# Performance work log

Hardware: AMD Instinct MI355X
Metric: run time of the kernel (lower is better)

Reference implementation:

```python
import jax, jax.numpy as jnp
import numpy as np

N_NODES = 100000
N_EDGES = 3200000
N_GRAPHS = 64
IN_FEATS = 128
NUM_CLASSES = 10


def setup_inputs() -> dict:
    key = jax.random.key(0)
    ks = jax.random.split(key, 12)
    in_feat = jax.random.normal(ks[0], (N_NODES, IN_FEATS), dtype=jnp.float32)
    src = jax.random.randint(ks[1], (N_EDGES,), 0, N_NODES, dtype=jnp.int32)
    dst = jax.random.randint(ks[2], (N_EDGES,), 0, N_NODES, dtype=jnp.int32)
    graph_ids = jnp.sort(jax.random.randint(ks[3], (N_NODES,), 0, N_GRAPHS, dtype=jnp.int32))
    def glorot(k, fan_in, fan_out):
        s = jnp.sqrt(6.0 / (fan_in + fan_out))
        return jax.random.uniform(k, (fan_in, fan_out), jnp.float32, -s, s)
    W1 = glorot(ks[4], IN_FEATS, 64); b1 = jnp.zeros((64,), jnp.float32)
    W2 = glorot(ks[5], 64, 128);      b2 = jnp.zeros((128,), jnp.float32)
    W3 = glorot(ks[6], 128, 64);      b3 = jnp.zeros((64,), jnp.float32)
    Wd = glorot(ks[7], 64, NUM_CLASSES)
    bd = jnp.zeros((NUM_CLASSES,), jnp.float32)
    return {"in_feat": in_feat, "src": src, "dst": dst, "graph_ids": graph_ids,
            "W1": W1, "b1": b1, "W2": W2, "b2": b2, "W3": W3, "b3": b3,
            "Wd": Wd, "bd": bd}


def _graph_conv(h, src, dst, norm_src, norm_dst, W, b):
    # DGL GraphConv, norm='both': h' = D_in^{-1/2} A (D_out^{-1/2} h) W + b
    x = h * norm_src[:, None]
    m = jax.ops.segment_sum(x[src], dst, num_segments=N_NODES)
    m = m * norm_dst[:, None]
    return m @ W + b


def reference(in_feat, src, dst, graph_ids, W1, b1, W2, b2, W3, b3, Wd, bd):
    ones = jnp.ones((N_EDGES,), jnp.float32)
    deg_out = jax.ops.segment_sum(ones, src, num_segments=N_NODES)
    deg_in = jax.ops.segment_sum(ones, dst, num_segments=N_NODES)
    norm_src = jax.lax.rsqrt(jnp.clip(deg_out, 1.0))
    norm_dst = jax.lax.rsqrt(jnp.clip(deg_in, 1.0))

    h = jax.nn.relu(_graph_conv(in_feat, src, dst, norm_src, norm_dst, W1, b1))
    h = jax.nn.relu(_graph_conv(h, src, dst, norm_src, norm_dst, W2, b2))
    h = jax.nn.relu(_graph_conv(h, src, dst, norm_src, norm_dst, W3, b3))

    hg = jax.ops.segment_sum(h, graph_ids, num_segments=N_GRAPHS)  # [G, 64]
    hg = jnp.tanh(hg)
    return hg @ Wd + bd  # [G, num_classes]
```

## Files before the change

### kernel.cpp

```cpp
#include <hip/hip_runtime.h>
#include <hip/hip_bf16.h>


constexpr int NN = 100000;
constexpr int NE = 3200000;
constexpr int NG = 64;

constexpr int CBITS = 16;
constexpr int CHUNK = 1 << CBITS;
constexpr int NCHUNK = (NE + CHUNK - 1) / CHUNK;
constexpr int WORDS4 = NN / 8;

typedef __attribute__((ext_vector_type(8))) short short8;
typedef __attribute__((ext_vector_type(4))) float f32x4;
typedef __attribute__((ext_vector_type(2))) float f32x2;


__global__ __launch_bounds__(1024) void hist_kernel(
    const int* __restrict__ src, const int* __restrict__ dst,
    uint* __restrict__ pdst, uint* __restrict__ psrc,
    unsigned char* __restrict__ lrank) {
  __shared__ uint bins[WORDS4];
  for (int i = threadIdx.x; i < WORDS4; i += 1024) bins[i] = 0;
  __syncthreads();
  const int c = blockIdx.x;
  const int start = c << CBITS;
  const int end = min(start + CHUNK, NE);
  if (blockIdx.y == 0) {
    for (int i = start + threadIdx.x; i < end; i += 1024) {
      int n = dst[i];
      uint old = atomicAdd(&bins[n >> 3], 1u << ((n & 7) * 4));
      lrank[i] = (unsigned char)((old >> ((n & 7) * 4)) & 0xf);
    }
  } else {
    for (int i = start + threadIdx.x; i < end; i += 1024) {
      int n = src[i];
      atomicAdd(&bins[n >> 3], 1u << ((n & 7) * 4));
    }
  }
  __syncthreads();
  uint* pp = ((blockIdx.y == 0) ? pdst : psrc) + (size_t)c * WORDS4;
  for (int i = threadIdx.x; i < WORDS4; i += 1024) pp[i] = bins[i];
}


__global__ __launch_bounds__(256) void reduce2_kernel(
    const uint* __restrict__ pdst, const uint* __restrict__ psrc,
    unsigned char* __restrict__ Pb, int* __restrict__ deg_in,
    float* __restrict__ nd, float* __restrict__ ns, float* __restrict__ hg) {
  int w = blockIdx.x * 256 + threadIdx.x;
  uint run[8] = {0, 0, 0, 0, 0, 0, 0, 0};
  if (blockIdx.y == 0) {
    if (w >= WORDS4) return;
#pragma unroll 7
    for (int c = 0; c < NCHUNK; ++c) {
      uint lo = run[0] | (run[1] << 8) | (run[2] << 16) | (run[3] << 24);
      uint hi = run[4] | (run[5] << 8) | (run[6] << 16) | (run[7] << 24);
      ((uint2*)(Pb + (size_t)c * NN))[w] = make_uint2(lo, hi);
      uint v = pdst[(size_t)c * WORDS4 + w];
#pragma unroll
      for (int k = 0; k < 8; ++k) run[k] += (v >> (4 * k)) & 0xfu;
    }
    ((int4*)deg_in)[2 * w] = make_int4(run[0], run[1], run[2], run[3]);
    ((int4*)deg_in)[2 * w + 1] = make_int4(run[4], run[5], run[6], run[7]);
    float4 f0, f1;
    f0.x = rsqrtf(fmaxf((float)run[0], 1.f));
    f0.y = rsqrtf(fmaxf((float)run[1], 1.f));
    f0.z = rsqrtf(fmaxf((float)run[2], 1.f));
    f0.w = rsqrtf(fmaxf((float)run[3], 1.f));
    f1.x = rsqrtf(fmaxf((float)run[4], 1.f));
    f1.y = rsqrtf(fmaxf((float)run[5], 1.f));
    f1.z = rsqrtf(fmaxf((float)run[6], 1.f));
    f1.w = rsqrtf(fmaxf((float)run[7], 1.f));
    ((float4*)nd)[2 * w] = f0;
    ((float4*)nd)[2 * w + 1] = f1;
  } else {
    if (blockIdx.x == 0) {
      for (int k = threadIdx.x; k < 1024; k += 256)
        ((float4*)hg)[k] = make_float4(0.f, 0.f, 0.f, 0.f);
    }
    if (w >= WORDS4) return;
#pragma unroll 7
    for (int c = 0; c < NCHUNK; ++c) {
      uint v = psrc[(size_t)c * WORDS4 + w];
#pragma unroll
      for (int k = 0; k < 8; ++k) run[k] += (v >> (4 * k)) & 0xfu;
    }
    float4 f0, f1;
    f0.x = rsqrtf(fmaxf((float)run[0], 1.f));
    f0.y = rsqrtf(fmaxf((float)run[1], 1.f));
    f0.z = rsqrtf(fmaxf((float)run[2], 1.f));
    f0.w = rsqrtf(fmaxf((float)run[3], 1.f));
    f1.x = rsqrtf(fmaxf((float)run[4], 1.f));
    f1.y = rsqrtf(fmaxf((float)run[5], 1.f));
    f1.z = rsqrtf(fmaxf((float)run[6], 1.f));
    f1.w = rsqrtf(fmaxf((float)run[7], 1.f));
    ((float4*)ns)[2 * w] = f0;
    ((float4*)ns)[2 * w + 1] = f1;
  }
}


__device__ __forceinline__ uint pack_bf16(float a, float b) {
  uint ua = __float_as_uint(a), ub = __float_as_uint(b);
  ua = (ua + 0x7fffu + ((ua >> 16) & 1u)) >> 16;
  ub = (ub + 0x7fffu + ((ub >> 16) & 1u)) & 0xffff0000u;
  return ua | ub;
}

__device__ __forceinline__ ushort to_bf16(float a) {
  uint ua = __float_as_uint(a);
  return (ushort)((ua + 0x7fffu + ((ua >> 16) & 1u)) >> 16);
}

union U16 {
  uint4 u;
  short8 s;
};
__device__ __forceinline__ short8 as_short8(uint4 u) {
  U16 t;
  t.u = u;
  return t.s;
}

__device__ __forceinline__ f32x2 bf2(uint u) {
  f32x2 r;
  r.x = __uint_as_float(u << 16);
  r.y = __uint_as_float(u & 0xffff0000u);
  return r;
}

__device__ __forceinline__ void add8(f32x2* a, uint4 v) {
  a[0] += bf2(v.x);
  a[1] += bf2(v.y);
  a[2] += bf2(v.z);
  a[3] += bf2(v.w);
}


__global__ __launch_bounds__(256) void scan1t_kernel(
    const int* __restrict__ deg, int* __restrict__ row_off,
    int* __restrict__ bsums, int n, const float* __restrict__ W1,
    const float* __restrict__ W2, const float* __restrict__ W3,
    ushort* __restrict__ Wt1, ushort* __restrict__ Wt2,
    ushort* __restrict__ Wt3) {
  int gi = blockIdx.x * 256 + threadIdx.x;
  if (gi < 8192) {
    int nn = gi >> 7, k = gi & 127;
    Wt1[gi] = to_bf16(W1[k * 64 + nn]);
  } else if (gi < 16384) {
    int j = gi - 8192;
    int nn = j >> 6, k = j & 63;
    Wt2[j] = to_bf16(W2[k * 128 + nn]);
  } else if (gi < 24576) {
    int j = gi - 16384;
    int nn = j >> 7, k = j & 127;
    Wt3[j] = to_bf16(W3[k * 64 + nn]);
  }
  __shared__ int s[256];
  int t = threadIdx.x;
  int base = blockIdx.x * 1024 + t * 4;
  int v0 = 0, v1 = 0, v2 = 0, v3 = 0;
  if (base + 0 < n) v0 = deg[base + 0];
  if (base + 1 < n) v1 = deg[base + 1];
  if (base + 2 < n) v2 = deg[base + 2];
  if (base + 3 < n) v3 = deg[base + 3];
  int sum = v0 + v1 + v2 + v3;
  s[t] = sum;
  __syncthreads();
  for (int off = 1; off < 256; off <<= 1) {
    int x = (t >= off) ? s[t - off] : 0;
    __syncthreads();
    s[t] += x;
    __syncthreads();
  }
  int excl = s[t] - sum;
  if (t == 255) bsums[blockIdx.x] = s[255];
  if (base + 0 < n) row_off[base + 0] = excl;
  if (base + 1 < n) row_off[base + 1] = excl + v0;
  if (base + 2 < n) row_off[base + 2] = excl + v0 + v1;
  if (base + 3 < n) row_off[base + 3] = excl + v0 + v1 + v2;
}


__global__ __launch_bounds__(256) void scan23_kernel(
    int* __restrict__ row_off, const int* __restrict__ bsums, int nb, int n) {
  __shared__ int si[128], so[128];
  int t = threadIdx.x;
  if (t < 128) {
    int v = (t < nb) ? bsums[t] : 0;
    si[t] = v;
    so[t] = v;
  }
  __syncthreads();
  for (int off = 1; off < 128; off <<= 1) {
    int x = 0;
    if (t < 128 && t >= off) x = si[t - off];
    __syncthreads();
    if (t < 128) si[t] += x;
    __syncthreads();
  }
  int i = blockIdx.x * 256 + t;
  if (i < n) {
    int bk = i >> 10;
    row_off[i] += si[bk] - so[bk];
  }
  if (blockIdx.x == 0 && t == 0) row_off[n] = si[127];
}


__global__ __launch_bounds__(256) void fill_kernel(
    const int* __restrict__ src, const int* __restrict__ dst,
    const int* __restrict__ row_off, const unsigned char* __restrict__ Pb,
    const unsigned char* __restrict__ lrank, int* __restrict__ csr, int e) {
  int i = blockIdx.x * 256 + threadIdx.x;
  if (i < e) {
    int d = dst[i];
    int c = i >> CBITS;
    int pos = row_off[d] + (int)Pb[(size_t)c * NN + d] + (int)lrank[i];
    csr[pos] = src[i];
  }
}


__global__ __launch_bounds__(256) void gemm1_kernel(
    const float* __restrict__ A, const ushort* __restrict__ Wt,
    const float* __restrict__ scale, ushort* __restrict__ C, int n) {
  int wid = threadIdx.x >> 6, lane = threadIdx.x & 63;
  int r = lane & 15, quad = lane >> 4;
  int m16 = blockIdx.x * 64 + wid * 16;
  if (m16 >= n) return;
  int mc = min(m16 + r, n - 1);
  short8 a[4];
#pragma unroll
  for (int ks = 0; ks < 4; ++ks) {
    const float4* p = (const float4*)(A + (size_t)mc * 128 + ks * 32 + quad * 8);
    float4 x = p[0], y = p[1];
    uint4 u;
    u.x = pack_bf16(x.x, x.y);
    u.y = pack_bf16(x.z, x.w);
    u.z = pack_bf16(y.x, y.y);
    u.w = pack_bf16(y.z, y.w);
    a[ks] = as_short8(u);
  }
#pragma unroll
  for (int nt = 0; nt < 4; ++nt) {
    f32x4 acc = {0.f, 0.f, 0.f, 0.f};
#pragma unroll
    for (int ks = 0; ks < 4; ++ks) {
      short8 b = as_short8(
          *(const uint4*)(Wt + (size_t)(nt * 16 + r) * 128 + ks * 32 + quad * 8));
      acc = __builtin_amdgcn_mfma_f32_16x16x32_bf16(a[ks], b, acc, 0, 0, 0);
    }
#pragma unroll
    for (int reg = 0; reg < 4; ++reg) {
      int m = m16 + quad * 4 + reg;
      if (m < n) C[(size_t)m * 64 + nt * 16 + r] = to_bf16(acc[reg] * scale[m]);
    }
  }
}


__global__ __launch_bounds__(256) void gemm23_kernel(
    const ushort* __restrict__ m2, const ushort* __restrict__ Wt2,
    const float* __restrict__ b2, const float* __restrict__ ns,
    const ushort* __restrict__ Wt3, ushort* __restrict__ t3, int n) {
  __shared__ ushort sX[4][16][136];
  int wid = threadIdx.x >> 6, lane = threadIdx.x & 63;
  int r = lane & 15, quad = lane >> 4;
  int m16 = blockIdx.x * 64 + wid * 16;
  if (m16 >= n) return;
  int mc = min(m16 + r, n - 1);
  short8 a1[2];
#pragma unroll
  for (int ks = 0; ks < 2; ++ks)
    a1[ks] = as_short8(*(const uint4*)(m2 + (size_t)mc * 64 + ks * 32 + quad * 8));
  float nsv[4];
#pragma unroll
  for (int reg = 0; reg < 4; ++reg)
    nsv[reg] = ns[min(m16 + quad * 4 + reg, n - 1)];
#pragma unroll
  for (int nt = 0; nt < 8; ++nt) {
    f32x4 acc = {0.f, 0.f, 0.f, 0.f};
#pragma unroll
    for (int ks = 0; ks < 2; ++ks) {
      short8 b = as_short8(
          *(const uint4*)(Wt2 + (size_t)(nt * 16 + r) * 64 + ks * 32 + quad * 8));
      acc = __builtin_amdgcn_mfma_f32_16x16x32_bf16(a1[ks], b, acc, 0, 0, 0);
    }
    float bv = b2[nt * 16 + r];
#pragma unroll
    for (int reg = 0; reg < 4; ++reg) {
      float v = fmaxf(acc[reg] + bv, 0.f) * nsv[reg];
      sX[wid][quad * 4 + reg][nt * 16 + r] = to_bf16(v);
    }
  }
  short8 a2[4];
#pragma unroll
  for (int ks = 0; ks < 4; ++ks)
    a2[ks] = as_short8(*(const uint4*)(&sX[wid][r][ks * 32 + quad * 8]));
#pragma unroll
  for (int nt = 0; nt < 4; ++nt) {
    f32x4 acc = {0.f, 0.f, 0.f, 0.f};
#pragma unroll
    for (int ks = 0; ks < 4; ++ks) {
      short8 b = as_short8(
          *(const uint4*)(Wt3 + (size_t)(nt * 16 + r) * 128 + ks * 32 + quad * 8));
      acc = __builtin_amdgcn_mfma_f32_16x16x32_bf16(a2[ks], b, acc, 0, 0, 0);
    }
#pragma unroll
    for (int reg = 0; reg < 4; ++reg) {
      int m = m16 + quad * 4 + reg;
      if (m < n) t3[(size_t)m * 64 + nt * 16 + r] = to_bf16(acc[reg]);
    }
  }
}


__device__ __forceinline__ void gather2_bf16(const int* __restrict__ csr,
                                             const ushort* __restrict__ x,
                                             int rs, int rm, int re, int lane,
                                             f32x2* a0, f32x2* a1) {
  const int eg = lane >> 3;
  const int fl = lane & 7;
  for (int e0 = rs; e0 < re; e0 += 64) {
    int idx = e0 + lane;
    int sv = (idx < re) ? csr[idx] : 0;
    int cnt = re - e0;
    if (cnt > 64) cnt = 64;
    int c0 = rm - e0;
#pragma unroll
    for (int j = 0; j < 8; ++j) {
      int jb = j * 8;
      if (jb < cnt) {
        int s = __shfl(sv, jb + eg);
        uint4 v = *(const uint4*)(x + (size_t)s * 64 + fl * 8);
        if (jb + 8 > cnt) {
          uint mv = ((jb + eg) < cnt) ? 0xffffffffu : 0u;
          v.x &= mv; v.y &= mv; v.z &= mv; v.w &= mv;
        }
        if (jb + 8 <= c0) {
          add8(a0, v);
        } else if (jb >= c0) {
          add8(a1, v);
        } else {
          uint m0 = ((jb + eg) < c0) ? 0xffffffffu : 0u;
          uint4 v0;
          v0.x = v.x & m0; v0.y = v.y & m0; v0.z = v.z & m0; v0.w = v.w & m0;
          add8(a0, v0);
          v.x ^= v0.x; v.y ^= v0.y; v.z ^= v0.z; v.w ^= v0.w;
          add8(a1, v);
        }
      }
    }
  }
#pragma unroll
  for (int k = 0; k < 4; ++k) {
    a0[k].x += __shfl_xor(a0[k].x, 8);
    a0[k].x += __shfl_xor(a0[k].x, 16);
    a0[k].x += __shfl_xor(a0[k].x, 32);
    a0[k].y += __shfl_xor(a0[k].y, 8);
    a0[k].y += __shfl_xor(a0[k].y, 16);
    a0[k].y += __shfl_xor(a0[k].y, 32);
    a1[k].x += __shfl_xor(a1[k].x, 8);
    a1[k].x += __shfl_xor(a1[k].x, 16);
    a1[k].x += __shfl_xor(a1[k].x, 32);
    a1[k].y += __shfl_xor(a1[k].y, 8);
    a1[k].y += __shfl_xor(a1[k].y, 16);
    a1[k].y += __shfl_xor(a1[k].y, 32);
  }
}

#define ACC_SEL(k) ((eg == 0) ? a0[(k) >> 1][(k)&1] : a1[(k) >> 1][(k)&1])


__global__ __launch_bounds__(256) void agg1_kernel(
    const int* __restrict__ row_off, const int* __restrict__ csr,
    const ushort* __restrict__ t, const float* __restrict__ nd,
    const float* __restrict__ ns, const float* __restrict__ b,
    ushort* __restrict__ out, int n) {
  int wid = threadIdx.x >> 6, lane = threadIdx.x & 63;
  int n0 = blockIdx.x * 8 + wid * 2;
  int rs = row_off[n0], rm = row_off[n0 + 1], re = row_off[n0 + 2];
  f32x2 a0[4] = {{0, 0}, {0, 0}, {0, 0}, {0, 0}};
  f32x2 a1[4] = {{0, 0}, {0, 0}, {0, 0}, {0, 0}};
  gather2_bf16(csr, t, rs, rm, re, lane, a0, a1);
  int eg = lane >> 3, fl = lane & 7;
  if (eg < 2) {
    int node = n0 + eg;
    float ndv = nd[node], nsv = ns[node];
    const float4* bp = (const float4*)(b + fl * 8);
    float4 b0 = bp[0], b1v = bp[1];
    float o0 = fmaxf(ACC_SEL(0) * ndv + b0.x, 0.f) * nsv;
    float o1 = fmaxf(ACC_SEL(1) * ndv + b0.y, 0.f) * nsv;
    float o2 = fmaxf(ACC_SEL(2) * ndv + b0.z, 0.f) * nsv;
    float o3 = fmaxf(ACC_SEL(3) * ndv + b0.w, 0.f) * nsv;
    float o4 = fmaxf(ACC_SEL(4) * ndv + b1v.x, 0.f) * nsv;
    float o5 = fmaxf(ACC_SEL(5) * ndv + b1v.y, 0.f) * nsv;
    float o6 = fmaxf(ACC_SEL(6) * ndv + b1v.z, 0.f) * nsv;
    float o7 = fmaxf(ACC_SEL(7) * ndv + b1v.w, 0.f) * nsv;
    uint4 v;
    v.x = pack_bf16(o0, o1);
    v.y = pack_bf16(o2, o3);
    v.z = pack_bf16(o4, o5);
    v.w = pack_bf16(o6, o7);
    *(uint4*)(out + (size_t)node * 64 + fl * 8) = v;
  }
}


__global__ __launch_bounds__(256) void agg2_kernel(
    const int* __restrict__ row_off, const int* __restrict__ csr,
    const ushort* __restrict__ h1s, const float* __restrict__ nd,
    ushort* __restrict__ m2, int n) {
  int wid = threadIdx.x >> 6, lane = threadIdx.x & 63;
  int n0 = blockIdx.x * 8 + wid * 2;
  int rs = row_off[n0], rm = row_off[n0 + 1], re = row_off[n0 + 2];
  f32x2 a0[4] = {{0, 0}, {0, 0}, {0, 0}, {0, 0}};
  f32x2 a1[4] = {{0, 0}, {0, 0}, {0, 0}, {0, 0}};
  gather2_bf16(csr, h1s, rs, rm, re, lane, a0, a1);
  int eg = lane >> 3, fl = lane & 7;
  if (eg < 2) {
    int node = n0 + eg;
    float ndv = nd[node];
    uint4 v;
    v.x = pack_bf16(ACC_SEL(0) * ndv, ACC_SEL(1) * ndv);
    v.y = pack_bf16(ACC_SEL(2) * ndv, ACC_SEL(3) * ndv);
    v.z = pack_bf16(ACC_SEL(4) * ndv, ACC_SEL(5) * ndv);
    v.w = pack_bf16(ACC_SEL(6) * ndv, ACC_SEL(7) * ndv);
    *(uint4*)(m2 + (size_t)node * 64 + fl * 8) = v;
  }
}


__global__ __launch_bounds__(512) void agg3_kernel(
    const int* __restrict__ row_off, const int* __restrict__ csr,
    const ushort* __restrict__ t, const float* __restrict__ nd,
    const float* __restrict__ b, const int* __restrict__ gid,
    float* __restrict__ hg, int n) {
  __shared__ float sO[16][64];
  __shared__ int sG[16];
  __shared__ int uni;
  int wid = threadIdx.x >> 6, lane = threadIdx.x & 63;
  int n0 = blockIdx.x * 16 + wid * 2;
  int rs = row_off[n0], rm = row_off[n0 + 1], re = row_off[n0 + 2];
  f32x2 a0[4] = {{0, 0}, {0, 0}, {0, 0}, {0, 0}};
  f32x2 a1[4] = {{0, 0}, {0, 0}, {0, 0}, {0, 0}};
  gather2_bf16(csr, t, rs, rm, re, lane, a0, a1);
  int eg = lane >> 3, fl = lane & 7;
  if (eg < 2) {
    int node = n0 + eg;
    int row = wid * 2 + eg;
    float ndv = nd[node];
    const float4* bp = (const float4*)(b + fl * 8);
    float4 b0 = bp[0], b1v = bp[1];
    sO[row][fl * 8 + 0] = fmaxf(ACC_SEL(0) * ndv + b0.x, 0.f);
    sO[row][fl * 8 + 1] = fmaxf(ACC_SEL(1) * ndv + b0.y, 0.f);
    sO[row][fl * 8 + 2] = fmaxf(ACC_SEL(2) * ndv + b0.z, 0.f);
    sO[row][fl * 8 + 3] = fmaxf(ACC_SEL(3) * ndv + b0.w, 0.f);
    sO[row][fl * 8 + 4] = fmaxf(ACC_SEL(4) * ndv + b1v.x, 0.f);
    sO[row][fl * 8 + 5] = fmaxf(ACC_SEL(5) * ndv + b1v.y, 0.f);
    sO[row][fl * 8 + 6] = fmaxf(ACC_SEL(6) * ndv + b1v.z, 0.f);
    sO[row][fl * 8 + 7] = fmaxf(ACC_SEL(7) * ndv + b1v.w, 0.f);
  }
  if (lane == 0) sG[wid * 2] = gid[n0];
  if (lane == 8) sG[wid * 2 + 1] = gid[n0 + 1];
  __syncthreads();
  if (threadIdx.x == 0) {
    int g0 = sG[0], u = 1;
#pragma unroll
    for (int i = 1; i < 16; ++i) u &= (sG[i] == g0);
    uni = u;
  }
  __syncthreads();
  if (uni) {
    int r = threadIdx.x >> 6;
#pragma unroll
    for (int s = 8; s >= 1; s >>= 1) {
      if (r < s) sO[r][lane] += sO[r + s][lane];
      __syncthreads();
    }
    if (threadIdx.x < 64) atomicAdd(&hg[sG[0] * 64 + lane], sO[0][lane]);
  } else {
    atomicAdd(&hg[sG[wid * 2] * 64 + lane], sO[wid * 2][lane]);
    atomicAdd(&hg[sG[wid * 2 + 1] * 64 + lane], sO[wid * 2 + 1][lane]);
  }
}


__global__ __launch_bounds__(640) void readout_kernel(
    const float* __restrict__ hg, const float* __restrict__ Wd,
    const float* __restrict__ bd, float* __restrict__ out) {
  int t = threadIdx.x;
  int g = t / 10, c = t % 10;
  float o = bd[c];
#pragma unroll 8
  for (int k = 0; k < 64; ++k) o += tanhf(hg[g * 64 + k]) * Wd[k * 10 + c];
  out[t] = o;
}


extern "C" void kernel_launch(void* const* d_in, const int* in_sizes, int n_in,
                              void* d_out, int out_size, void* d_ws, size_t ws_size,
                              hipStream_t stream) {
  const float* in_feat = (const float*)d_in[0];
  const int* src = (const int*)d_in[1];
  const int* dst = (const int*)d_in[2];
  const int* gid = (const int*)d_in[3];
  const float* W1 = (const float*)d_in[4];
  const float* b1 = (const float*)d_in[5];
  const float* W2 = (const float*)d_in[6];
  const float* b2 = (const float*)d_in[7];
  const float* W3 = (const float*)d_in[8];
  const float* b3 = (const float*)d_in[9];
  const float* Wd = (const float*)d_in[10];
  const float* bd = (const float*)d_in[11];
  float* out = (float*)d_out;

  char* ws = (char*)d_ws;
  size_t o = 0;
  auto alloc = [&](size_t bytes) -> char* {
    char* p = ws + o;
    o = (o + bytes + 1023) & ~(size_t)1023;
    return p;
  };
  float* hg = (float*)alloc(NG * 64 * 4);
  int* deg_in = (int*)alloc(NN * 4);
  float* norm_src = (float*)alloc(NN * 4);
  float* norm_dst = (float*)alloc(NN * 4);
  int* row_off = (int*)alloc((NN + 1) * 4);
  int* bsums = (int*)alloc(512);
  ushort* Wt1 = (ushort*)alloc(64 * 128 * 2);
  ushort* Wt2 = (ushort*)alloc(128 * 64 * 2);
  ushort* Wt3 = (ushort*)alloc(64 * 128 * 2);
  int* csr = (int*)alloc((size_t)NE * 4);
  ushort* tbuf = (ushort*)alloc((size_t)NN * 64 * 2);
  ushort* h1s = (ushort*)alloc((size_t)NN * 64 * 2);
  ushort* m2 = (ushort*)alloc((size_t)NN * 64 * 2);
  (void)ws_size;

  char* ov = (char*)tbuf;
  uint* pdst = (uint*)ov;
  uint* psrc = (uint*)(ov + 2457600);
  unsigned char* Pb = (unsigned char*)(ov + 4915200);
  unsigned char* lrank = (unsigned char*)(ov + 9830400);

  const int egrid = (NE + 255) / 256;
  const int ngrid = (NN + 255) / 256;
  const int sgrid = (NN + 1023) / 1024;
  const int wgrid2 = NN / 8;
  const int rgrid = (WORDS4 + 255) / 256;
  const int ggrid = (NN + 63) / 64;

  hist_kernel<<<dim3(NCHUNK, 2), 1024, 0, stream>>>(src, dst, pdst, psrc, lrank);
  reduce2_kernel<<<dim3(rgrid, 2), 256, 0, stream>>>(pdst, psrc, Pb, deg_in,
                                                     norm_dst, norm_src, hg);
  scan1t_kernel<<<sgrid, 256, 0, stream>>>(deg_in, row_off, bsums, NN, W1, W2,
                                           W3, Wt1, Wt2, Wt3);
  scan23_kernel<<<ngrid, 256, 0, stream>>>(row_off, bsums, sgrid, NN);
  fill_kernel<<<egrid, 256, 0, stream>>>(src, dst, row_off, Pb, lrank, csr, NE);

  gemm1_kernel<<<ggrid, 256, 0, stream>>>(in_feat, Wt1, norm_src, tbuf, NN);
  agg1_kernel<<<wgrid2, 256, 0, stream>>>(row_off, csr, tbuf, norm_dst,
                                          norm_src, b1, h1s, NN);
  agg2_kernel<<<wgrid2, 256, 0, stream>>>(row_off, csr, h1s, norm_dst, m2, NN);
  gemm23_kernel<<<ggrid, 256, 0, stream>>>(m2, Wt2, b2, norm_src, Wt3, tbuf, NN);
  agg3_kernel<<<NN / 16, 512, 0, stream>>>(row_off, csr, tbuf, norm_dst, b3,
                                           gid, hg, NN);
  readout_kernel<<<1, 640, 0, stream>>>(hg, Wd, bd, out);
}
```

Before: 447.7 us.

## Replace chunked-histogram CSR build with a two-pass bucket sort by destination

```diff
diff --git a/kernel.cpp b/kernel.cpp
--- a/kernel.cpp
+++ b/kernel.cpp
@@ -11,93 +11,31 @@
 constexpr int NCHUNK = (NE + CHUNK - 1) / CHUNK;
 constexpr int WORDS4 = NN / 8;
 
+constexpr int NBK = 196;
+constexpr int BCAP = 18000;
+constexpr int NBA = 100;
+constexpr int EPB = 32000;
+
 typedef __attribute__((ext_vector_type(8))) short short8;
 typedef __attribute__((ext_vector_type(4))) float f32x4;
 typedef __attribute__((ext_vector_type(2))) float f32x2;
 
 
-__global__ __launch_bounds__(1024) void hist_kernel(
-    const int* __restrict__ src, const int* __restrict__ dst,
-    uint* __restrict__ pdst, uint* __restrict__ psrc,
-    unsigned char* __restrict__ lrank) {
+__global__ __launch_bounds__(1024) void histsrc_kernel(
+    const int* __restrict__ src, uint* __restrict__ psrc) {
   __shared__ uint bins[WORDS4];
   for (int i = threadIdx.x; i < WORDS4; i += 1024) bins[i] = 0;
   __syncthreads();
   const int c = blockIdx.x;
   const int start = c << CBITS;
   const int end = min(start + CHUNK, NE);
-  if (blockIdx.y == 0) {
-    for (int i = start + threadIdx.x; i < end; i += 1024) {
-      int n = dst[i];
-      uint old = atomicAdd(&bins[n >> 3], 1u << ((n & 7) * 4));
-      lrank[i] = (unsigned char)((old >> ((n & 7) * 4)) & 0xf);
-    }
-  } else {
-    for (int i = start + threadIdx.x; i < end; i += 1024) {
-      int n = src[i];
-      atomicAdd(&bins[n >> 3], 1u << ((n & 7) * 4));
-    }
-  }
-  __syncthreads();
-  uint* pp = ((blockIdx.y == 0) ? pdst : psrc) + (size_t)c * WORDS4;
+  for (int i = start + threadIdx.x; i < end; i += 1024) {
+    int n = src[i];
+    atomicAdd(&bins[n >> 3], 1u << ((n & 7) * 4));
+  }
+  __syncthreads();
+  uint* pp = psrc + (size_t)c * WORDS4;
   for (int i = threadIdx.x; i < WORDS4; i += 1024) pp[i] = bins[i];
-}
-
-
-__global__ __launch_bounds__(256) void reduce2_kernel(
-    const uint* __restrict__ pdst, const uint* __restrict__ psrc,
-    unsigned char* __restrict__ Pb, int* __restrict__ deg_in,
-    float* __restrict__ nd, float* __restrict__ ns, float* __restrict__ hg) {
-  int w = blockIdx.x * 256 + threadIdx.x;
-  uint run[8] = {0, 0, 0, 0, 0, 0, 0, 0};
-  if (blockIdx.y == 0) {
-    if (w >= WORDS4) return;
-#pragma unroll 7
-    for (int c = 0; c < NCHUNK; ++c) {
-      uint lo = run[0] | (run[1] << 8) | (run[2] << 16) | (run[3] << 24);
-      uint hi = run[4] | (run[5] << 8) | (run[6] << 16) | (run[7] << 24);
-      ((uint2*)(Pb + (size_t)c * NN))[w] = make_uint2(lo, hi);
-      uint v = pdst[(size_t)c * WORDS4 + w];
-#pragma unroll
-      for (int k = 0; k < 8; ++k) run[k] += (v >> (4 * k)) & 0xfu;
-    }
-    ((int4*)deg_in)[2 * w] = make_int4(run[0], run[1], run[2], run[3]);
-    ((int4*)deg_in)[2 * w + 1] = make_int4(run[4], run[5], run[6], run[7]);
-    float4 f0, f1;
-    f0.x = rsqrtf(fmaxf((float)run[0], 1.f));
-    f0.y = rsqrtf(fmaxf((float)run[1], 1.f));
-    f0.z = rsqrtf(fmaxf((float)run[2], 1.f));
-    f0.w = rsqrtf(fmaxf((float)run[3], 1.f));
-    f1.x = rsqrtf(fmaxf((float)run[4], 1.f));
-    f1.y = rsqrtf(fmaxf((float)run[5], 1.f));
-    f1.z = rsqrtf(fmaxf((float)run[6], 1.f));
-    f1.w = rsqrtf(fmaxf((float)run[7], 1.f));
-    ((float4*)nd)[2 * w] = f0;
-    ((float4*)nd)[2 * w + 1] = f1;
-  } else {
-    if (blockIdx.x == 0) {
-      for (int k = threadIdx.x; k < 1024; k += 256)
-        ((float4*)hg)[k] = make_float4(0.f, 0.f, 0.f, 0.f);
-    }
-    if (w >= WORDS4) return;
-#pragma unroll 7
-    for (int c = 0; c < NCHUNK; ++c) {
-      uint v = psrc[(size_t)c * WORDS4 + w];
-#pragma unroll
-      for (int k = 0; k < 8; ++k) run[k] += (v >> (4 * k)) & 0xfu;
-    }
-    float4 f0, f1;
-    f0.x = rsqrtf(fmaxf((float)run[0], 1.f));
-    f0.y = rsqrtf(fmaxf((float)run[1], 1.f));
-    f0.z = rsqrtf(fmaxf((float)run[2], 1.f));
-    f0.w = rsqrtf(fmaxf((float)run[3], 1.f));
-    f1.x = rsqrtf(fmaxf((float)run[4], 1.f));
-    f1.y = rsqrtf(fmaxf((float)run[5], 1.f));
-    f1.z = rsqrtf(fmaxf((float)run[6], 1.f));
-    f1.w = rsqrtf(fmaxf((float)run[7], 1.f));
-    ((float4*)ns)[2 * w] = f0;
-    ((float4*)ns)[2 * w + 1] = f1;
-  }
 }
 
 
@@ -138,12 +76,12 @@
 }
 
 
-__global__ __launch_bounds__(256) void scan1t_kernel(
-    const int* __restrict__ deg, int* __restrict__ row_off,
-    int* __restrict__ bsums, int n, const float* __restrict__ W1,
-    const float* __restrict__ W2, const float* __restrict__ W3,
-    ushort* __restrict__ Wt1, ushort* __restrict__ Wt2,
-    ushort* __restrict__ Wt3) {
+__global__ __launch_bounds__(256) void reduce_ns_kernel(
+    const uint* __restrict__ psrc, float* __restrict__ ns,
+    const float* __restrict__ W1, const float* __restrict__ W2,
+    const float* __restrict__ W3, ushort* __restrict__ Wt1,
+    ushort* __restrict__ Wt2, ushort* __restrict__ Wt3,
+    float* __restrict__ hg, int* __restrict__ cursor) {
   int gi = blockIdx.x * 256 + threadIdx.x;
   if (gi < 8192) {
     int nn = gi >> 7, k = gi & 127;
@@ -157,68 +95,114 @@
     int nn = j >> 7, k = j & 127;
     Wt3[j] = to_bf16(W3[k * 64 + nn]);
   }
-  __shared__ int s[256];
-  int t = threadIdx.x;
-  int base = blockIdx.x * 1024 + t * 4;
-  int v0 = 0, v1 = 0, v2 = 0, v3 = 0;
-  if (base + 0 < n) v0 = deg[base + 0];
-  if (base + 1 < n) v1 = deg[base + 1];
-  if (base + 2 < n) v2 = deg[base + 2];
-  if (base + 3 < n) v3 = deg[base + 3];
-  int sum = v0 + v1 + v2 + v3;
-  s[t] = sum;
+  if (blockIdx.x == 95) {
+    for (int k = threadIdx.x; k < 1024; k += 256)
+      ((float4*)hg)[k] = make_float4(0.f, 0.f, 0.f, 0.f);
+    for (int k = threadIdx.x; k < NBK; k += 256) cursor[k] = 0;
+    return;
+  }
+  int w = gi;
+  if (w >= WORDS4) return;
+  uint run[8] = {0, 0, 0, 0, 0, 0, 0, 0};
+#pragma unroll 7
+  for (int c = 0; c < NCHUNK; ++c) {
+    uint v = psrc[(size_t)c * WORDS4 + w];
+#pragma unroll
+    for (int k = 0; k < 8; ++k) run[k] += (v >> (4 * k)) & 0xfu;
+  }
+  float4 f0, f1;
+  f0.x = rsqrtf(fmaxf((float)run[0], 1.f));
+  f0.y = rsqrtf(fmaxf((float)run[1], 1.f));
+  f0.z = rsqrtf(fmaxf((float)run[2], 1.f));
+  f0.w = rsqrtf(fmaxf((float)run[3], 1.f));
+  f1.x = rsqrtf(fmaxf((float)run[4], 1.f));
+  f1.y = rsqrtf(fmaxf((float)run[5], 1.f));
+  f1.z = rsqrtf(fmaxf((float)run[6], 1.f));
+  f1.w = rsqrtf(fmaxf((float)run[7], 1.f));
+  ((float4*)ns)[2 * w] = f0;
+  ((float4*)ns)[2 * w + 1] = f1;
+}
+
+
+__global__ __launch_bounds__(1024) void bucketA_kernel(
+    const int* __restrict__ src, const int* __restrict__ dst,
+    int* __restrict__ cursor, int2* __restrict__ pairs) {
+  __shared__ int cnt[NBK];
+  __shared__ int gb[NBK];
+  for (int i = threadIdx.x; i < NBK; i += 1024) cnt[i] = 0;
+  __syncthreads();
+  const int start = blockIdx.x * EPB;
+  const int end = start + EPB;
+  for (int i = start + threadIdx.x; i < end; i += 1024)
+    atomicAdd(&cnt[dst[i] >> 9], 1);
+  __syncthreads();
+  for (int i = threadIdx.x; i < NBK; i += 1024)
+    gb[i] = atomicAdd(&cursor[i], cnt[i]);
+  __syncthreads();
+  for (int i = threadIdx.x; i < NBK; i += 1024) cnt[i] = 0;
+  __syncthreads();
+  for (int i = start + threadIdx.x; i < end; i += 1024) {
+    int d = dst[i];
+    int b = d >> 9;
+    int r = gb[b] + atomicAdd(&cnt[b], 1);
+    if (r < BCAP) pairs[(size_t)b * BCAP + r] = make_int2(src[i], d);
+  }
+}
+
+
+__global__ __launch_bounds__(1024) void bucketB_kernel(
+    const int* __restrict__ cursor, const int2* __restrict__ pairs,
+    int* __restrict__ row_off, float* __restrict__ nd,
+    int* __restrict__ csr) {
+  __shared__ int sc[256];
+  __shared__ int rowloc[512];
+  __shared__ int rank[512];
+  const int b = blockIdx.x;
+  const int t = threadIdx.x;
+  if (t < 256) sc[t] = (t < NBK) ? min(cursor[t], BCAP) : 0;
   __syncthreads();
   for (int off = 1; off < 256; off <<= 1) {
-    int x = (t >= off) ? s[t - off] : 0;
+    int x = 0;
+    if (t < 256 && t >= off) x = sc[t - off];
     __syncthreads();
-    s[t] += x;
+    if (t < 256) sc[t] += x;
     __syncthreads();
   }
-  int excl = s[t] - sum;
-  if (t == 255) bsums[blockIdx.x] = s[255];
-  if (base + 0 < n) row_off[base + 0] = excl;
-  if (base + 1 < n) row_off[base + 1] = excl + v0;
-  if (base + 2 < n) row_off[base + 2] = excl + v0 + v1;
-  if (base + 3 < n) row_off[base + 3] = excl + v0 + v1 + v2;
-}
-
-
-__global__ __launch_bounds__(256) void scan23_kernel(
-    int* __restrict__ row_off, const int* __restrict__ bsums, int nb, int n) {
-  __shared__ int si[128], so[128];
-  int t = threadIdx.x;
-  if (t < 128) {
-    int v = (t < nb) ? bsums[t] : 0;
-    si[t] = v;
-    so[t] = v;
-  }
-  __syncthreads();
-  for (int off = 1; off < 128; off <<= 1) {
+  const int base = (b == 0) ? 0 : sc[b - 1];
+  const int cnt_b = min(cursor[b], BCAP);
+  if (t < 512) rank[t] = 0;
+  __syncthreads();
+  for (int i = t; i < cnt_b; i += 1024)
+    atomicAdd(&rank[pairs[(size_t)b * BCAP + i].y & 511], 1);
+  __syncthreads();
+  if (t < 512) rowloc[t] = rank[t];
+  __syncthreads();
+  for (int off = 1; off < 512; off <<= 1) {
     int x = 0;
-    if (t < 128 && t >= off) x = si[t - off];
+    if (t < 512 && t >= off) x = rowloc[t - off];
     __syncthreads();
-    if (t < 128) si[t] += x;
+    if (t < 512) rowloc[t] += x;
     __syncthreads();
   }
-  int i = blockIdx.x * 256 + t;
-  if (i < n) {
-    int bk = i >> 10;
-    row_off[i] += si[bk] - so[bk];
-  }
-  if (blockIdx.x == 0 && t == 0) row_off[n] = si[127];
-}
-
-
-__global__ __launch_bounds__(256) void fill_kernel(
-    const int* __restrict__ src, const int* __restrict__ dst,
-    const int* __restrict__ row_off, const unsigned char* __restrict__ Pb,
-    const unsigned char* __restrict__ lrank, int* __restrict__ csr, int e) {
-  int i = blockIdx.x * 256 + threadIdx.x;
-  if (i < e) {
-    int d = dst[i];
-    int c = i >> CBITS;
-    int pos = row_off[d] + (int)Pb[(size_t)c * NN + d] + (int)lrank[i];
-    csr[pos] = src[i];
+  const int nlo = b << 9;
+  const int nodes = min(512, NN - nlo);
+  int deg = 0;
+  if (t < 512) deg = rank[t];
+  if (t < nodes) {
+    row_off[nlo + t] = base + rowloc[t] - deg;
+    nd[nlo + t] = rsqrtf(fmaxf((float)deg, 1.0f));
+  }
+  if (b == NBK - 1 && t == 0) row_off[NN] = base + cnt_b;
+  __syncthreads();
+  if (t < 512) rowloc[t] -= deg;
+  __syncthreads();
+  if (t < 512) rank[t] = 0;
+  __syncthreads();
+  for (int i = t; i < cnt_b; i += 1024) {
+    int2 p = pairs[(size_t)b * BCAP + i];
+    int dl = p.y & 511;
+    int r = atomicAdd(&rank[dl], 1);
+    csr[base + rowloc[dl] + r] = p.x;
   }
 }
 
@@ -525,11 +509,10 @@
     return p;
   };
   float* hg = (float*)alloc(NG * 64 * 4);
-  int* deg_in = (int*)alloc(NN * 4);
+  int* cursor = (int*)alloc(NBK * 4);
   float* norm_src = (float*)alloc(NN * 4);
   float* norm_dst = (float*)alloc(NN * 4);
   int* row_off = (int*)alloc((NN + 1) * 4);
-  int* bsums = (int*)alloc(512);
   ushort* Wt1 = (ushort*)alloc(64 * 128 * 2);
   ushort* Wt2 = (ushort*)alloc(128 * 64 * 2);
   ushort* Wt3 = (ushort*)alloc(64 * 128 * 2);
@@ -540,25 +523,18 @@
   (void)ws_size;
 
   char* ov = (char*)tbuf;
-  uint* pdst = (uint*)ov;
-  uint* psrc = (uint*)(ov + 2457600);
-  unsigned char* Pb = (unsigned char*)(ov + 4915200);
-  unsigned char* lrank = (unsigned char*)(ov + 9830400);
-
-  const int egrid = (NE + 255) / 256;
-  const int ngrid = (NN + 255) / 256;
-  const int sgrid = (NN + 1023) / 1024;
+  uint* psrc = (uint*)ov;
+  int2* pairs = (int2*)(ov + 2457600);
+
   const int wgrid2 = NN / 8;
-  const int rgrid = (WORDS4 + 255) / 256;
   const int ggrid = (NN + 63) / 64;
 
-  hist_kernel<<<dim3(NCHUNK, 2), 1024, 0, stream>>>(src, dst, pdst, psrc, lrank);
-  reduce2_kernel<<<dim3(rgrid, 2), 256, 0, stream>>>(pdst, psrc, Pb, deg_in,
-                                                     norm_dst, norm_src, hg);
-  scan1t_kernel<<<sgrid, 256, 0, stream>>>(deg_in, row_off, bsums, NN, W1, W2,
-                                           W3, Wt1, Wt2, Wt3);
-  scan23_kernel<<<ngrid, 256, 0, stream>>>(row_off, bsums, sgrid, NN);
-  fill_kernel<<<egrid, 256, 0, stream>>>(src, dst, row_off, Pb, lrank, csr, NE);
+  histsrc_kernel<<<NCHUNK, 1024, 0, stream>>>(src, psrc);
+  reduce_ns_kernel<<<96, 256, 0, stream>>>(psrc, norm_src, W1, W2, W3, Wt1,
+                                           Wt2, Wt3, hg, cursor);
+  bucketA_kernel<<<NBA, 1024, 0, stream>>>(src, dst, cursor, pairs);
+  bucketB_kernel<<<NBK, 1024, 0, stream>>>(cursor, pairs, row_off, norm_dst,
+                                           csr);
 
   gemm1_kernel<<<ggrid, 256, 0, stream>>>(in_feat, Wt1, norm_src, tbuf, NN);
   agg1_kernel<<<wgrid2, 256, 0, stream>>>(row_off, csr, tbuf, norm_dst,
```

New measurement: 463.8 us. 3.6% more time.
